# Kernel tuning notes

Measured on AMD Instinct MI355X. Metric: run time of the kernel, lower is better.

Reference implementation:

```python
import math
import jax, jax.numpy as jnp
import numpy as np

B, C, M = 32, 1024, 1024
D, DV, R_ANCHOR = 512, 512, 64


def setup_inputs() -> dict:
    key = jax.random.key(0)
    ks = jax.random.split(key, 6)
    return {
        "T": jax.random.normal(ks[0], (B, C, M), dtype=jnp.float32),
        "Wq": jax.random.normal(ks[1], (C, D), dtype=jnp.float32) * 0.02,
        "Wk": jax.random.normal(ks[2], (C, D), dtype=jnp.float32) * 0.02,
        "Wv": jax.random.normal(ks[3], (C, DV), dtype=jnp.float32) * 0.02,
        "Wout": jax.random.normal(ks[4], (DV, C), dtype=jnp.float32) * 0.02,
        "R_full": jax.random.normal(ks[5], (R_ANCHOR, M), dtype=jnp.float32) * 0.02,
    }


def reference(T, Wq, Wk, Wv, Wout, R_full):
    # T: [B, C, m] -> tokens-major [B, m, C]
    b, c, m = T.shape
    T_mC = jnp.swapaxes(T, 1, 2)
    Q = T_mC @ Wq           # [B, m, D]
    K = T_mC @ Wk           # [B, m, D]
    V = T_mC @ Wv           # [B, m, DV]
    Rm = R_full[:, :m]      # [r, m]
    # Faithful to original torch einsum: m and j are summed INDEPENDENTLY
    # (outer product of row-sums of R with token-sums of K/V), not contracted.
    K_proj = jnp.einsum('rm,bjd->brd', Rm, K)   # [B, r, D]
    V_proj = jnp.einsum('rm,bjd->brd', Rm, V)   # [B, r, DV]
    scale = 1.0 / math.sqrt(max(1.0, float(Wq.shape[1])))
    scores = jnp.einsum('bid,btd->bit', Q, K_proj) * scale  # [B, m, r]
    A = jax.nn.softmax(scores, axis=-1)
    T_out_mdv = jnp.einsum('bir,brd->bid', A, V_proj)       # [B, m, DV]
    T_out_C = T_out_mdv @ Wout                               # [B, m, C]
    return jnp.swapaxes(T_out_C, 1, 2)                       # [B, C, m]
```

## Files before the change

kernel.cpp:

```cpp
#include <hip/hip_runtime.h>
#include <math.h>

constexpr int Bc  = 32;
constexpr int Cc  = 1024;
constexpr int Mc  = 1024;
constexpr int Dc  = 512;
constexpr int DVc = 512;
constexpr int Rc  = 64;

typedef float f4 __attribute__((ext_vector_type(4)));

__global__ __launch_bounds__(512) void k_kv1(const float* __restrict__ T,
                                             const float* __restrict__ Wk,
                                             const float* __restrict__ Wv,
                                             float* __restrict__ pK,
                                             float* __restrict__ pV) {
    __shared__ float ts[64];
    const int cs  = blockIdx.x;
    const int b   = blockIdx.y;
    const int c0  = cs * 64;
    const int tid = threadIdx.x;
    const int w   = tid >> 6, lane = tid & 63;

    const float* Tb = T + ((long)b * Cc + c0) * Mc;
#pragma unroll 4
    for (int r = w * 8; r < w * 8 + 8; ++r) {
        const float* row = Tb + (long)r * Mc;
        float s = 0.f;
#pragma unroll
        for (int k = 0; k < 4; ++k) {
            float4 t = *(const float4*)&row[k * 256 + lane * 4];
            s += (t.x + t.y) + (t.z + t.w);
        }
#pragma unroll
        for (int off = 32; off; off >>= 1) s += __shfl_down(s, off, 64);
        if (lane == 0) ts[r] = s;
    }
    __syncthreads();

    const int d = tid;
    float k1 = 0.f, v1 = 0.f;
#pragma unroll 4
    for (int c = 0; c < 64; ++c) {
        float t = ts[c];
        k1 = fmaf(t, Wk[(long)(c0 + c) * Dc  + d], k1);
        v1 = fmaf(t, Wv[(long)(c0 + c) * DVc + d], v1);
    }
    const long base = ((long)b * 16 + cs) * 512;
    pK[base + d] = k1;
    pV[base + d] = v1;
}

__global__ __launch_bounds__(256) void k_kv2r(const float* __restrict__ pK,
                                              const float* __restrict__ pV,
                                              float* __restrict__ Ksum,
                                              float* __restrict__ Vsum,
                                              const float* __restrict__ Rfull,
                                              float* __restrict__ rsum) {
    if (blockIdx.x < 128) {
        const int gid = blockIdx.x * 256 + threadIdx.x;
        const int sel = gid >> 14;
        const int rem = gid & 16383;
        const float* p = (sel ? pV : pK) + (long)(rem >> 9) * 16 * 512 + (rem & 511);
        float s = 0.f;
#pragma unroll
        for (int i = 0; i < 16; ++i) s += p[i * 512];
        (sel ? Vsum : Ksum)[rem] = s;
    } else {
        const int row  = (blockIdx.x - 128) * 4 + (threadIdx.x >> 6);
        const int lane = threadIdx.x & 63;
        const float* xr = Rfull + (long)row * 1024;
        float s = 0.f;
#pragma unroll
        for (int k = 0; k < 4; ++k) {
            float4 t = *(const float4*)&xr[k * 256 + lane * 4];
            s += (t.x + t.y) + (t.z + t.w);
        }
#pragma unroll
        for (int off = 32; off; off >>= 1) s += __shfl_down(s, off, 64);
        if (lane == 0) rsum[row] = s;
    }
}

__global__ __launch_bounds__(256) void k_mid(const float* __restrict__ Wq,
                                             const float* __restrict__ Ksum,
                                             float* __restrict__ wqk,
                                             const float* __restrict__ Wout,
                                             const float* __restrict__ Vsum,
                                             float* __restrict__ pVW) {
    __shared__ float vs[64];
    if (blockIdx.x < 8192) {
        const int wid  = blockIdx.x * 4 + (threadIdx.x >> 6);
        const int lane = threadIdx.x & 63;
        const float* wq = Wq + (long)(wid & 1023) * Dc;
        const float* ks = Ksum + (wid >> 10) * Dc;
        float s = 0.f;
#pragma unroll
        for (int k = 0; k < 4; ++k) {
            int d = k * 128 + lane * 2;
            float2 a = *(const float2*)&wq[d];
            float2 x = *(const float2*)&ks[d];
            s = fmaf(a.x, x.x, s);
            s = fmaf(a.y, x.y, s);
        }
#pragma unroll
        for (int off = 32; off; off >>= 1) s += __shfl_down(s, off, 64);
        if (lane == 0) wqk[wid] = s;
    } else {
        const int idx = blockIdx.x - 8192;
        const int ds  = idx & 7;
        const int b   = idx >> 3;
        const int d0  = ds * 64;
        const int tid = threadIdx.x;
        if (tid < 64) vs[tid] = Vsum[b * Dc + d0 + tid];
        __syncthreads();
        float a0 = 0.f, a1 = 0.f, a2 = 0.f, a3 = 0.f;
        const float* W0 = Wout + (long)d0 * Cc + tid;
#pragma unroll 4
        for (int d = 0; d < 64; ++d) {
            float v = vs[d];
            const float* wr = W0 + (long)d * Cc;
            a0 = fmaf(v, wr[0],   a0);
            a1 = fmaf(v, wr[256], a1);
            a2 = fmaf(v, wr[512], a2);
            a3 = fmaf(v, wr[768], a3);
        }
        const long base = ((long)b * 8 + ds) * 1024 + tid;
        pVW[base] = a0;  pVW[base + 256] = a1;
        pVW[base + 512] = a2;  pVW[base + 768] = a3;
    }
}

__global__ __launch_bounds__(512) void k_final(const float* __restrict__ T,
                                               const float* __restrict__ wqk,
                                               const float* __restrict__ pVW,
                                               const float* __restrict__ rsum,
                                               float* __restrict__ Out,
                                               float scale) {
    __shared__ float rs[64];
    __shared__ float part[32][72];
    __shared__ float wsh[64];
    __shared__ float wql[Cc];
    __shared__ float vwl[Cc];

    const int b   = blockIdx.y;
    const int m0  = blockIdx.x * 64;
    const int tid = threadIdx.x;
    const int il  = tid & 15;
    const int cs  = tid >> 4;

    if (tid < 256) ((float4*)wql)[tid] = ((const float4*)(wqk + b * Cc))[tid];
#pragma unroll
    for (int c = tid; c < Cc; c += 512) {
        const float* p = pVW + (long)b * 8 * 1024 + c;
        float s = 0.f;
#pragma unroll
        for (int j = 0; j < 8; ++j) s += p[j * 1024];
        vwl[c] = s;
    }
    if (tid < 64) rs[tid] = rsum[tid];
    __syncthreads();

    const float* Tbm = T + (long)b * Cc * Mc + m0 + il * 4;

    float4 acc = make_float4(0.f, 0.f, 0.f, 0.f);
#pragma unroll 8
    for (int c = cs; c < Cc; c += 32) {
        float4 t = *(const float4*)&Tbm[(long)c * Mc];
        float wc = wql[c];
        acc.x = fmaf(t.x, wc, acc.x);
        acc.y = fmaf(t.y, wc, acc.y);
        acc.z = fmaf(t.z, wc, acc.z);
        acc.w = fmaf(t.w, wc, acc.w);
    }
    *(float4*)&part[cs][il * 4] = acc;
    __syncthreads();

    if (tid < 64) {
        const int i = tid;
        float q = 0.f;
#pragma unroll
        for (int k = 0; k < 32; ++k) q += part[k][i];
        q *= scale;
        float mx = -1e30f;
#pragma unroll
        for (int r = 0; r < 64; ++r) mx = fmaxf(mx, q * rs[r]);
        float se = 0.f, sw = 0.f;
#pragma unroll
        for (int r = 0; r < 64; ++r) {
            float e = __expf(q * rs[r] - mx);
            se += e;
            sw = fmaf(e, rs[r], sw);
        }
        wsh[i] = sw / se;
    }
    __syncthreads();

    float* Ob = Out + (long)b * Cc * Mc + m0 + il * 4;
    float4 w4 = *(const float4*)&wsh[il * 4];
#pragma unroll 4
    for (int c = cs; c < Cc; c += 32) {
        float v = vwl[c];
        f4 o = {w4.x * v, w4.y * v, w4.z * v, w4.w * v};
        __builtin_nontemporal_store(o, (f4*)&Ob[(long)c * Mc]);
    }
}

extern "C" void kernel_launch(void* const* d_in, const int* in_sizes, int n_in,
                              void* d_out, int out_size, void* d_ws, size_t ws_size,
                              hipStream_t stream) {
    const float* T     = (const float*)d_in[0];
    const float* Wq    = (const float*)d_in[1];
    const float* Wk    = (const float*)d_in[2];
    const float* Wv    = (const float*)d_in[3];
    const float* Wout  = (const float*)d_in[4];
    const float* Rfull = (const float*)d_in[5];
    float* Out = (float*)d_out;

    float* ws   = (float*)d_ws;
    float* rsum = ws;
    float* Ksum = rsum + Rc;
    float* Vsum = Ksum + Bc * Dc;
    float* wqk  = Vsum + Bc * DVc;
    float* vw   = wqk + Bc * Cc;
    float* pK   = vw + Bc * Cc;
    float* pV   = pK + 262144;
    float* pVW  = pV + 262144;

    k_kv1<<<dim3(16, Bc), 512, 0, stream>>>(T, Wk, Wv, pK, pV);
    k_kv2r<<<144, 256, 0, stream>>>(pK, pV, Ksum, Vsum, Rfull, rsum);
    k_mid<<<8448, 256, 0, stream>>>(Wq, Ksum, wqk, Wout, Vsum, pVW);
    const float scale = 1.0f / sqrtf((float)Dc);
    k_final<<<dim3(Mc / 64, Bc), 512, 0, stream>>>(T, wqk, pVW, rsum, Out, scale);
}
```

Baseline: 290.4 us.

## Fuse four kernels into one persistent kernel with atomic grid barriers

Replaces the four-kernel chain with a single 512-block kernel that runs the K/V partial sums, the Wq/Wout projections and the final softmax/output phase, separated by two software grid barriers built on an atomic counter that a tiny init kernel resets. Each block now recomputes the per-batch Ksum/Vsum reduction locally instead of reading it from a separate kernel, and the Wout partials are reduced in shared memory rather than through a global scratch buffer. The aim is to remove launch gaps and intermediate global round trips. In exchange it depends on all 512 blocks being co-resident (launch_bounds 512,4), spin-waits at the barriers, and adds redundant reduction work per block.

```diff
diff --git a/kernel.cpp b/kernel.cpp
--- a/kernel.cpp
+++ b/kernel.cpp
@@ -10,199 +10,192 @@
 
 typedef float f4 __attribute__((ext_vector_type(4)));
 
-__global__ __launch_bounds__(512) void k_kv1(const float* __restrict__ T,
-                                             const float* __restrict__ Wk,
-                                             const float* __restrict__ Wv,
-                                             float* __restrict__ pK,
-                                             float* __restrict__ pV) {
+__global__ void k_init(int* bar) { *bar = 0; }
+
+__device__ __forceinline__ void grid_sync(int* bar, int target) {
+    __syncthreads();
+    if (threadIdx.x == 0) {
+        __threadfence();
+        __hip_atomic_fetch_add(bar, 1, __ATOMIC_RELEASE, __HIP_MEMORY_SCOPE_AGENT);
+        while (__hip_atomic_load(bar, __ATOMIC_ACQUIRE, __HIP_MEMORY_SCOPE_AGENT) < target)
+            __builtin_amdgcn_s_sleep(2);
+    }
+    __syncthreads();
+    __threadfence();
+}
+
+__global__ __launch_bounds__(512, 4) void k_mega(
+    const float* __restrict__ T,    const float* __restrict__ Wq,
+    const float* __restrict__ Wk,   const float* __restrict__ Wv,
+    const float* __restrict__ Wout, const float* __restrict__ Rfull,
+    float* __restrict__ Out,
+    float* __restrict__ pK, float* __restrict__ pV,
+    float* __restrict__ wqk, float* __restrict__ vw,
+    float* __restrict__ rsum, int* bar, float scale) {
+
     __shared__ float ts[64];
-    const int cs  = blockIdx.x;
-    const int b   = blockIdx.y;
-    const int c0  = cs * 64;
-    const int tid = threadIdx.x;
-    const int w   = tid >> 6, lane = tid & 63;
-
-    const float* Tb = T + ((long)b * Cc + c0) * Mc;
-#pragma unroll 4
-    for (int r = w * 8; r < w * 8 + 8; ++r) {
-        const float* row = Tb + (long)r * Mc;
-        float s = 0.f;
-#pragma unroll
-        for (int k = 0; k < 4; ++k) {
-            float4 t = *(const float4*)&row[k * 256 + lane * 4];
-            s += (t.x + t.y) + (t.z + t.w);
-        }
-#pragma unroll
-        for (int off = 32; off; off >>= 1) s += __shfl_down(s, off, 64);
-        if (lane == 0) ts[r] = s;
-    }
-    __syncthreads();
-
-    const int d = tid;
-    float k1 = 0.f, v1 = 0.f;
-#pragma unroll 4
-    for (int c = 0; c < 64; ++c) {
-        float t = ts[c];
-        k1 = fmaf(t, Wk[(long)(c0 + c) * Dc  + d], k1);
-        v1 = fmaf(t, Wv[(long)(c0 + c) * DVc + d], v1);
-    }
-    const long base = ((long)b * 16 + cs) * 512;
-    pK[base + d] = k1;
-    pV[base + d] = v1;
-}
-
-__global__ __launch_bounds__(256) void k_kv2r(const float* __restrict__ pK,
-                                              const float* __restrict__ pV,
-                                              float* __restrict__ Ksum,
-                                              float* __restrict__ Vsum,
-                                              const float* __restrict__ Rfull,
-                                              float* __restrict__ rsum) {
-    if (blockIdx.x < 128) {
-        const int gid = blockIdx.x * 256 + threadIdx.x;
-        const int sel = gid >> 14;
-        const int rem = gid & 16383;
-        const float* p = (sel ? pV : pK) + (long)(rem >> 9) * 16 * 512 + (rem & 511);
-        float s = 0.f;
-#pragma unroll
-        for (int i = 0; i < 16; ++i) s += p[i * 512];
-        (sel ? Vsum : Ksum)[rem] = s;
-    } else {
-        const int row  = (blockIdx.x - 128) * 4 + (threadIdx.x >> 6);
-        const int lane = threadIdx.x & 63;
-        const float* xr = Rfull + (long)row * 1024;
-        float s = 0.f;
-#pragma unroll
-        for (int k = 0; k < 4; ++k) {
-            float4 t = *(const float4*)&xr[k * 256 + lane * 4];
-            s += (t.x + t.y) + (t.z + t.w);
-        }
-#pragma unroll
-        for (int off = 32; off; off >>= 1) s += __shfl_down(s, off, 64);
-        if (lane == 0) rsum[row] = s;
-    }
-}
-
-__global__ __launch_bounds__(256) void k_mid(const float* __restrict__ Wq,
-                                             const float* __restrict__ Ksum,
-                                             float* __restrict__ wqk,
-                                             const float* __restrict__ Wout,
-                                             const float* __restrict__ Vsum,
-                                             float* __restrict__ pVW) {
-    __shared__ float vs[64];
-    if (blockIdx.x < 8192) {
-        const int wid  = blockIdx.x * 4 + (threadIdx.x >> 6);
-        const int lane = threadIdx.x & 63;
-        const float* wq = Wq + (long)(wid & 1023) * Dc;
-        const float* ks = Ksum + (wid >> 10) * Dc;
-        float s = 0.f;
-#pragma unroll
-        for (int k = 0; k < 4; ++k) {
-            int d = k * 128 + lane * 2;
-            float2 a = *(const float2*)&wq[d];
-            float2 x = *(const float2*)&ks[d];
-            s = fmaf(a.x, x.x, s);
-            s = fmaf(a.y, x.y, s);
-        }
-#pragma unroll
-        for (int off = 32; off; off >>= 1) s += __shfl_down(s, off, 64);
-        if (lane == 0) wqk[wid] = s;
-    } else {
-        const int idx = blockIdx.x - 8192;
-        const int ds  = idx & 7;
-        const int b   = idx >> 3;
-        const int d0  = ds * 64;
-        const int tid = threadIdx.x;
-        if (tid < 64) vs[tid] = Vsum[b * Dc + d0 + tid];
-        __syncthreads();
-        float a0 = 0.f, a1 = 0.f, a2 = 0.f, a3 = 0.f;
-        const float* W0 = Wout + (long)d0 * Cc + tid;
-#pragma unroll 4
-        for (int d = 0; d < 64; ++d) {
-            float v = vs[d];
-            const float* wr = W0 + (long)d * Cc;
-            a0 = fmaf(v, wr[0],   a0);
-            a1 = fmaf(v, wr[256], a1);
-            a2 = fmaf(v, wr[512], a2);
-            a3 = fmaf(v, wr[768], a3);
-        }
-        const long base = ((long)b * 8 + ds) * 1024 + tid;
-        pVW[base] = a0;  pVW[base + 256] = a1;
-        pVW[base + 512] = a2;  pVW[base + 768] = a3;
-    }
-}
-
-__global__ __launch_bounds__(512) void k_final(const float* __restrict__ T,
-                                               const float* __restrict__ wqk,
-                                               const float* __restrict__ pVW,
-                                               const float* __restrict__ rsum,
-                                               float* __restrict__ Out,
-                                               float scale) {
+    __shared__ float Ks[512];
+    __shared__ float Vs[512];
+    __shared__ float pb[8][64];
     __shared__ float rs[64];
     __shared__ float part[32][72];
     __shared__ float wsh[64];
     __shared__ float wql[Cc];
     __shared__ float vwl[Cc];
 
-    const int b   = blockIdx.y;
-    const int m0  = blockIdx.x * 64;
-    const int tid = threadIdx.x;
-    const int il  = tid & 15;
-    const int cs  = tid >> 4;
-
-    if (tid < 256) ((float4*)wql)[tid] = ((const float4*)(wqk + b * Cc))[tid];
-#pragma unroll
-    for (int c = tid; c < Cc; c += 512) {
-        const float* p = pVW + (long)b * 8 * 1024 + c;
-        float s = 0.f;
-#pragma unroll
-        for (int j = 0; j < 8; ++j) s += p[j * 1024];
-        vwl[c] = s;
-    }
-    if (tid < 64) rs[tid] = rsum[tid];
-    __syncthreads();
-
-    const float* Tbm = T + (long)b * Cc * Mc + m0 + il * 4;
-
-    float4 acc = make_float4(0.f, 0.f, 0.f, 0.f);
+    const int tid  = threadIdx.x;
+    const int w    = tid >> 6;
+    const int lane = tid & 63;
+
+    {
+        const int cs = blockIdx.x & 15;
+        const int b  = blockIdx.x >> 4;
+        const int c0 = cs * 64;
+        const float* Tb = T + ((long)b * Cc + c0) * Mc;
+#pragma unroll 4
+        for (int r = w * 8; r < w * 8 + 8; ++r) {
+            const float* row = Tb + (long)r * Mc;
+            float s = 0.f;
+#pragma unroll
+            for (int k = 0; k < 4; ++k) {
+                float4 t = *(const float4*)&row[k * 256 + lane * 4];
+                s += (t.x + t.y) + (t.z + t.w);
+            }
+#pragma unroll
+            for (int off = 32; off; off >>= 1) s += __shfl_down(s, off, 64);
+            if (lane == 0) ts[r] = s;
+        }
+        __syncthreads();
+
+        const int d = tid;
+        float k1 = 0.f, v1 = 0.f;
+#pragma unroll 4
+        for (int c = 0; c < 64; ++c) {
+            float t = ts[c];
+            k1 = fmaf(t, Wk[(long)(c0 + c) * Dc  + d], k1);
+            v1 = fmaf(t, Wv[(long)(c0 + c) * DVc + d], v1);
+        }
+        const long base = ((long)b * 16 + cs) * 512;
+        pK[base + d] = k1;
+        pV[base + d] = v1;
+    }
+
+    grid_sync(bar, 512);
+
+    {
+        const int b   = blockIdx.x >> 4;
+        const int csl = blockIdx.x & 15;
+        const int c0  = csl * 64;
+
+        {
+            const float* pKb = pK + (long)b * 16 * 512 + tid;
+            const float* pVb = pV + (long)b * 16 * 512 + tid;
+            float a = 0.f, c2 = 0.f;
+#pragma unroll
+            for (int i = 0; i < 16; ++i) { a += pKb[i * 512]; c2 += pVb[i * 512]; }
+            Ks[tid] = a; Vs[tid] = c2;
+        }
+
+        if (blockIdx.x < 64 && w == 0) {
+            const float* xr = Rfull + (long)blockIdx.x * Mc;
+            float s = 0.f;
+#pragma unroll
+            for (int k = 0; k < 4; ++k) {
+                float4 t = *(const float4*)&xr[k * 256 + lane * 4];
+                s += (t.x + t.y) + (t.z + t.w);
+            }
+#pragma unroll
+            for (int off = 32; off; off >>= 1) s += __shfl_down(s, off, 64);
+            if (lane == 0) rsum[blockIdx.x] = s;
+        }
+        __syncthreads();
+
+        for (int j = 0; j < 8; ++j) {
+            const int c = c0 + w * 8 + j;
+            const float* wq = Wq + (long)c * Dc;
+            float s = 0.f;
+#pragma unroll
+            for (int k = 0; k < 8; ++k)
+                s = fmaf(wq[lane + k * 64], Ks[lane + k * 64], s);
+#pragma unroll
+            for (int off = 32; off; off >>= 1) s += __shfl_down(s, off, 64);
+            if (lane == 0) wqk[b * Cc + c] = s;
+        }
+
+        {
+            float acc = 0.f;
+            const int dbase = w * 64;
 #pragma unroll 8
-    for (int c = cs; c < Cc; c += 32) {
-        float4 t = *(const float4*)&Tbm[(long)c * Mc];
-        float wc = wql[c];
-        acc.x = fmaf(t.x, wc, acc.x);
-        acc.y = fmaf(t.y, wc, acc.y);
-        acc.z = fmaf(t.z, wc, acc.z);
-        acc.w = fmaf(t.w, wc, acc.w);
-    }
-    *(float4*)&part[cs][il * 4] = acc;
-    __syncthreads();
-
-    if (tid < 64) {
-        const int i = tid;
-        float q = 0.f;
-#pragma unroll
-        for (int k = 0; k < 32; ++k) q += part[k][i];
-        q *= scale;
-        float mx = -1e30f;
-#pragma unroll
-        for (int r = 0; r < 64; ++r) mx = fmaxf(mx, q * rs[r]);
-        float se = 0.f, sw = 0.f;
-#pragma unroll
-        for (int r = 0; r < 64; ++r) {
-            float e = __expf(q * rs[r] - mx);
-            se += e;
-            sw = fmaf(e, rs[r], sw);
-        }
-        wsh[i] = sw / se;
-    }
-    __syncthreads();
-
-    float* Ob = Out + (long)b * Cc * Mc + m0 + il * 4;
-    float4 w4 = *(const float4*)&wsh[il * 4];
+            for (int dd = 0; dd < 64; ++dd) {
+                const int d = dbase + dd;
+                acc = fmaf(Vs[d], Wout[(long)d * Cc + c0 + lane], acc);
+            }
+            pb[w][lane] = acc;
+        }
+        __syncthreads();
+        if (tid < 64) {
+            float s = 0.f;
+#pragma unroll
+            for (int i = 0; i < 8; ++i) s += pb[i][tid];
+            vw[b * Cc + c0 + tid] = s;
+        }
+    }
+
+    grid_sync(bar, 1024);
+
+    {
+        const int b  = blockIdx.x >> 4;
+        const int m0 = (blockIdx.x & 15) * 64;
+        const int il = tid & 15;
+        const int cs = tid >> 4;
+
+        if (tid < 256)       ((float4*)wql)[tid]       = ((const float4*)(wqk + b * Cc))[tid];
+        else                 ((float4*)vwl)[tid - 256] = ((const float4*)(vw  + b * Cc))[tid - 256];
+        if (tid < 64) rs[tid] = rsum[tid];
+        __syncthreads();
+
+        const float* Tbm = T + (long)b * Cc * Mc + m0 + il * 4;
+        float4 acc = make_float4(0.f, 0.f, 0.f, 0.f);
+#pragma unroll 8
+        for (int c = cs; c < Cc; c += 32) {
+            float4 t = *(const float4*)&Tbm[(long)c * Mc];
+            float wc = wql[c];
+            acc.x = fmaf(t.x, wc, acc.x);
+            acc.y = fmaf(t.y, wc, acc.y);
+            acc.z = fmaf(t.z, wc, acc.z);
+            acc.w = fmaf(t.w, wc, acc.w);
+        }
+        *(float4*)&part[cs][il * 4] = acc;
+        __syncthreads();
+
+        if (tid < 64) {
+            const int i = tid;
+            float q = 0.f;
+#pragma unroll
+            for (int k = 0; k < 32; ++k) q += part[k][i];
+            q *= scale;
+            float mx = -1e30f;
+#pragma unroll
+            for (int r = 0; r < 64; ++r) mx = fmaxf(mx, q * rs[r]);
+            float se = 0.f, sw = 0.f;
+#pragma unroll
+            for (int r = 0; r < 64; ++r) {
+                float e = __expf(q * rs[r] - mx);
+                se += e;
+                sw = fmaf(e, rs[r], sw);
+            }
+            wsh[i] = sw / se;
+        }
+        __syncthreads();
+
+        float* Ob = Out + (long)b * Cc * Mc + m0 + il * 4;
+        float4 w4 = *(const float4*)&wsh[il * 4];
 #pragma unroll 4
-    for (int c = cs; c < Cc; c += 32) {
-        float v = vwl[c];
-        f4 o = {w4.x * v, w4.y * v, w4.z * v, w4.w * v};
-        __builtin_nontemporal_store(o, (f4*)&Ob[(long)c * Mc]);
+        for (int c = cs; c < Cc; c += 32) {
+            float v = vwl[c];
+            f4 o = {w4.x * v, w4.y * v, w4.z * v, w4.w * v};
+            __builtin_nontemporal_store(o, (f4*)&Ob[(long)c * Mc]);
+        }
     }
 }
 
@@ -225,11 +218,10 @@
     float* vw   = wqk + Bc * Cc;
     float* pK   = vw + Bc * Cc;
     float* pV   = pK + 262144;
-    float* pVW  = pV + 262144;
-
-    k_kv1<<<dim3(16, Bc), 512, 0, stream>>>(T, Wk, Wv, pK, pV);
-    k_kv2r<<<144, 256, 0, stream>>>(pK, pV, Ksum, Vsum, Rfull, rsum);
-    k_mid<<<8448, 256, 0, stream>>>(Wq, Ksum, wqk, Wout, Vsum, pVW);
+    int*   bar  = (int*)(pV + 262144);
+
     const float scale = 1.0f / sqrtf((float)Dc);
-    k_final<<<dim3(Mc / 64, Bc), 512, 0, stream>>>(T, wqk, pVW, rsum, Out, scale);
+    k_init<<<1, 1, 0, stream>>>(bar);
+    k_mega<<<512, 512, 0, stream>>>(T, Wq, Wk, Wv, Wout, Rfull, Out,
+                                    pK, pV, wqk, vw, rsum, bar, scale);
 }
```

After: 508.9 us. +75.2%, slower.
